# Kernel tuning notes

Hardware: AMD Instinct MI355X
Metric: run time of the kernel (lower is better)

The kernel has to match this reference:

```python
import jax, jax.numpy as jnp
import numpy as np

B, T, IN, H = 16, 4096, 512, 512


def gru_layer(x, W_ih, W_hh, b_ih, b_hh):
    """Single-layer batch_first GRU, torch gate ordering (r, z, n), h0 = 0.
    x: [B, T, IN]; W_ih: [3H, IN]; W_hh: [3H, H]; b_ih, b_hh: [3H].
    Returns outputs [B, T, H]."""
    Bn = x.shape[0]
    Hn = W_hh.shape[1]
    # input-side gate pre-activations computed once as a big GEMM
    xg = jnp.einsum('bti,gi->btg', x, W_ih) + b_ih  # [B, T, 3H]

    def step(h, xg_t):
        hg = h @ W_hh.T + b_hh  # [B, 3H]
        xr, xz, xn = jnp.split(xg_t, 3, axis=-1)
        hr, hz, hn = jnp.split(hg, 3, axis=-1)
        r = jax.nn.sigmoid(xr + hr)
        z = jax.nn.sigmoid(xz + hz)
        n = jnp.tanh(xn + r * hn)
        h_new = (1.0 - z) * n + z * h
        return h_new, h_new

    h0 = jnp.zeros((Bn, Hn), dtype=x.dtype)
    _, ys = jax.lax.scan(step, h0, jnp.swapaxes(xg, 0, 1))  # [T, B, H]
    return jnp.swapaxes(ys, 0, 1)


def setup_inputs() -> dict:
    key = jax.random.key(0)
    ks = jax.random.split(key, 9)
    s = 1.0 / np.sqrt(H)  # torch GRU init scale
    x = jax.random.normal(ks[0], (B, T, IN), dtype=jnp.float32)
    W_ih1 = jax.random.uniform(ks[1], (3 * H, IN), jnp.float32, -s, s)
    W_hh1 = jax.random.uniform(ks[2], (3 * H, H), jnp.float32, -s, s)
    b_ih1 = jax.random.uniform(ks[3], (3 * H,), jnp.float32, -s, s)
    b_hh1 = jax.random.uniform(ks[4], (3 * H,), jnp.float32, -s, s)
    W_ih2 = jax.random.uniform(ks[5], (3 * H, H), jnp.float32, -s, s)
    W_hh2 = jax.random.uniform(ks[6], (3 * H, H), jnp.float32, -s, s)
    b_ih2 = jax.random.uniform(ks[7], (3 * H,), jnp.float32, -s, s)
    b_hh2 = jax.random.uniform(ks[8], (3 * H,), jnp.float32, -s, s)
    return {"x": x, "W_ih1": W_ih1, "W_hh1": W_hh1, "b_ih1": b_ih1, "b_hh1": b_hh1,
            "W_ih2": W_ih2, "W_hh2": W_hh2, "b_ih2": b_ih2, "b_hh2": b_hh2}


def reference(x, W_ih1, W_hh1, b_ih1, b_hh1, W_ih2, W_hh2, b_ih2, b_hh2):
    y = gru_layer(x, W_ih1, W_hh1, b_ih1, b_hh1)  # rnn1
    z = gru_layer(y, W_ih2, W_hh2, b_ih2, b_hh2)  # rnn2
    return z + y  # residual skip around second GRU
```

## Files before the change

### kernel.cpp

```cpp
#include <hip/hip_runtime.h>
#include <hip/hip_bf16.h>


namespace {

constexpr int BATCH = 16;
constexpr int SEQ   = 4096;
constexpr int HD    = 512;
constexpr int NWG_L = 32;
constexpr int SLICE = 16;
constexpr int RING  = 8;
constexpr int BLK   = 6 * 64;

typedef short bf16x8 __attribute__((ext_vector_type(8)));
typedef float f32x4  __attribute__((ext_vector_type(4)));

__device__ __forceinline__ unsigned short f2bf(float f) {
  unsigned u = __float_as_uint(f);
  return (unsigned short)((u + 0x7fffu + ((u >> 16) & 1u)) >> 16);
}
__device__ __forceinline__ float bf2f(unsigned short s) {
  return __uint_as_float(((unsigned)s) << 16);
}

__device__ __forceinline__ void wait_ge(const unsigned* f, unsigned tgt) {
  while (__hip_atomic_load(f, __ATOMIC_RELAXED, __HIP_MEMORY_SCOPE_AGENT) < tgt) {}
}

#define MFMA16(a, b, c) __builtin_amdgcn_mfma_f32_16x16x32_bf16((a), (b), (c), 0, 0, 0)

__global__ __launch_bounds__(BLK, 1) void gru2_kernel(
    const float* __restrict__ x,
    const float* __restrict__ Wih1, const float* __restrict__ Whh1,
    const float* __restrict__ bih1, const float* __restrict__ bhh1,
    const float* __restrict__ Wih2, const float* __restrict__ Whh2,
    const float* __restrict__ bih2, const float* __restrict__ bhh2,
    float* __restrict__ out,
    unsigned* flags,
    unsigned short* ring)
{
  const int wg    = blockIdx.x;
  const int layer = wg >> 5;
  const int g     = wg & 31;
  const int tid   = threadIdx.x;
  const int w     = tid >> 6;
  const int lane  = tid & 63;
  const int nidx  = lane & 15;
  const int kgrp  = lane >> 4;

  __shared__ float gate_buf[6][16][16];
  __shared__ float h_own[16][16];

  const float* Wih = layer ? Wih2 : Wih1;
  const float* Whh = layer ? Whh2 : Whh1;
  const float* bih = layer ? bih2 : bih1;
  const float* bhh = layer ? bhh2 : bhh1;

  unsigned* flags1    = flags;
  unsigned* flags2    = flags + 32;
  unsigned* flags_own = layer ? flags2 : flags1;

  const unsigned short* ring1 = ring;
  unsigned short* ring_own = ring + (size_t)layer * (RING * BATCH * HD);

  if (tid < 256) h_own[tid >> 4][tid & 15] = 0.f;

  const int gate = (w < 3) ? w : (w - 3);
  const float* Wmat = (w < 3) ? Wih : Whh;
  const float* wrow = Wmat + ((size_t)gate * HD + (size_t)g * SLICE + nidx) * HD + kgrp * 8;
  bf16x8 bfrag[16];
  #pragma unroll
  for (int kk = 0; kk < 16; ++kk) {
    const float* p = wrow + kk * 32;
    bf16x8 f;
    #pragma unroll
    for (int i = 0; i < 8; ++i) f[i] = (short)f2bf(p[i]);
    bfrag[kk] = f;
  }

  float bi_r = 0, bi_z = 0, bi_n = 0, bh_r = 0, bh_z = 0, bh_n = 0;
  if (tid < 256) {
    int u = g * SLICE + (tid & 15);
    bi_r = bih[u]; bi_z = bih[HD + u]; bi_n = bih[2 * HD + u];
    bh_r = bhh[u]; bh_z = bhh[HD + u]; bh_n = bhh[2 * HD + u];
  }
  __syncthreads();

  for (int t = 0; t < SEQ; ++t) {
    f32x4 ac0 = {0.f,0.f,0.f,0.f}, ac1 = {0.f,0.f,0.f,0.f};
    f32x4 ac2 = {0.f,0.f,0.f,0.f}, ac3 = {0.f,0.f,0.f,0.f};

    if (w < 3) {
      if (layer == 0) {
        const float* px = x + ((size_t)nidx * SEQ + t) * HD + kgrp * 8;
        #pragma unroll
        for (int kk = 0; kk < 16; ++kk) {
          const float* p = px + kk * 32;
          bf16x8 a;
          #pragma unroll
          for (int i = 0; i < 8; ++i) a[i] = (short)f2bf(p[i]);
          if ((kk & 3) == 0)      ac0 = MFMA16(a, bfrag[kk], ac0);
          else if ((kk & 3) == 1) ac1 = MFMA16(a, bfrag[kk], ac1);
          else if ((kk & 3) == 2) ac2 = MFMA16(a, bfrag[kk], ac2);
          else                    ac3 = MFMA16(a, bfrag[kk], ac3);
        }
      } else {
        if (lane < 32) wait_ge(&flags1[lane], (unsigned)(t + 1));
        __builtin_amdgcn_fence(__ATOMIC_ACQUIRE, "agent");
        const unsigned short* py =
            ring1 + ((size_t)(t & (RING - 1)) * BATCH + nidx) * HD + kgrp * 8;
        #pragma unroll
        for (int kk = 0; kk < 16; ++kk) {
          bf16x8 a = *(const bf16x8*)(py + kk * 32);
          if ((kk & 3) == 0)      ac0 = MFMA16(a, bfrag[kk], ac0);
          else if ((kk & 3) == 1) ac1 = MFMA16(a, bfrag[kk], ac1);
          else if ((kk & 3) == 2) ac2 = MFMA16(a, bfrag[kk], ac2);
          else                    ac3 = MFMA16(a, bfrag[kk], ac3);
        }
      }
    } else {
      if (t > 0) {
        if (lane < 32) {
          wait_ge(&flags_own[lane], (unsigned)t);
        } else if (layer == 0 && t >= RING) {
          wait_ge(&flags2[lane - 32], (unsigned)(t - RING + 1));
        }
        __builtin_amdgcn_fence(__ATOMIC_ACQUIRE, "agent");
        const unsigned short* ph =
            ring_own + ((size_t)((t - 1) & (RING - 1)) * BATCH + nidx) * HD + kgrp * 8;
        #pragma unroll
        for (int kk = 0; kk < 16; ++kk) {
          bf16x8 a = *(const bf16x8*)(ph + kk * 32);
          if ((kk & 3) == 0)      ac0 = MFMA16(a, bfrag[kk], ac0);
          else if ((kk & 3) == 1) ac1 = MFMA16(a, bfrag[kk], ac1);
          else if ((kk & 3) == 2) ac2 = MFMA16(a, bfrag[kk], ac2);
          else                    ac3 = MFMA16(a, bfrag[kk], ac3);
        }
      }
    }

    f32x4 acc = (ac0 + ac1) + (ac2 + ac3);
    #pragma unroll
    for (int j = 0; j < 4; ++j) gate_buf[w][kgrp * 4 + j][nidx] = acc[j];
    __syncthreads();

    if (tid < 256) {
      const int b = tid >> 4, u = tid & 15;
      float rp = gate_buf[0][b][u] + bi_r + gate_buf[3][b][u] + bh_r;
      float zp = gate_buf[1][b][u] + bi_z + gate_buf[4][b][u] + bh_z;
      float xn = gate_buf[2][b][u] + bi_n;
      float hn = gate_buf[5][b][u] + bh_n;
      float r = 1.f / (1.f + __expf(-rp));
      float z = 1.f / (1.f + __expf(-zp));
      float n = tanhf(xn + r * hn);
      float hp = h_own[b][u];
      float hv = (1.f - z) * n + z * hp;
      h_own[b][u] = hv;
      ring_own[((size_t)(t & (RING - 1)) * BATCH + b) * HD + g * SLICE + u] = f2bf(hv);
      if (layer == 1) {
        float y = bf2f(ring1[((size_t)(t & (RING - 1)) * BATCH + b) * HD + g * SLICE + u]);
        out[((size_t)b * SEQ + t) * HD + g * SLICE + u] = hv + y;
      }
    }
    __syncthreads();
    if (tid == 0) {
      __builtin_amdgcn_fence(__ATOMIC_RELEASE, "agent");
      __hip_atomic_store(&flags_own[g], (unsigned)(t + 1),
                         __ATOMIC_RELAXED, __HIP_MEMORY_SCOPE_AGENT);
    }
  }
}

}

extern "C" void kernel_launch(void* const* d_in, const int* in_sizes, int n_in,
                              void* d_out, int out_size, void* d_ws, size_t ws_size,
                              hipStream_t stream) {
  const float* x    = (const float*)d_in[0];
  const float* Wih1 = (const float*)d_in[1];
  const float* Whh1 = (const float*)d_in[2];
  const float* bih1 = (const float*)d_in[3];
  const float* bhh1 = (const float*)d_in[4];
  const float* Wih2 = (const float*)d_in[5];
  const float* Whh2 = (const float*)d_in[6];
  const float* bih2 = (const float*)d_in[7];
  const float* bhh2 = (const float*)d_in[8];

  unsigned* flags = (unsigned*)d_ws;
  unsigned short* ring = (unsigned short*)((char*)d_ws + 1024);

  hipMemsetAsync(d_ws, 0, 1024, stream);

  gru2_kernel<<<dim3(2 * NWG_L), dim3(BLK), 0, stream>>>(
      x, Wih1, Whh1, bih1, bhh1, Wih2, Whh2, bih2, bhh2,
      (float*)d_out, flags, ring);
}
```

Measured before the change: 37.12 ms.

## Rewrite GRU pipeline with tagged-data rings, wider slices and LDS staging

Result: slower. 58.83 ms (+58.5%).

```diff
diff --git a/kernel.cpp b/kernel.cpp
--- a/kernel.cpp
+++ b/kernel.cpp
@@ -7,13 +7,16 @@
 constexpr int BATCH = 16;
 constexpr int SEQ   = 4096;
 constexpr int HD    = 512;
-constexpr int NWG_L = 32;
-constexpr int SLICE = 16;
-constexpr int RING  = 8;
-constexpr int BLK   = 6 * 64;
-
-typedef short bf16x8 __attribute__((ext_vector_type(8)));
-typedef float f32x4  __attribute__((ext_vector_type(4)));
+constexpr int NSLOT = 128;
+constexpr int NWGL  = 16;
+constexpr int SLICE = 32;
+constexpr int BLK   = 384;
+constexpr int SLOTU = BATCH * HD;
+
+typedef short    bf16x8 __attribute__((ext_vector_type(8)));
+typedef float    f32x4  __attribute__((ext_vector_type(4)));
+typedef unsigned u32x4  __attribute__((ext_vector_type(4)));
+typedef short    s16x4  __attribute__((ext_vector_type(4)));
 
 __device__ __forceinline__ unsigned short f2bf(float f) {
   unsigned u = __float_as_uint(f);
@@ -22,153 +25,285 @@
 __device__ __forceinline__ float bf2f(unsigned short s) {
   return __uint_as_float(((unsigned)s) << 16);
 }
-
-__device__ __forceinline__ void wait_ge(const unsigned* f, unsigned tgt) {
-  while (__hip_atomic_load(f, __ATOMIC_RELAXED, __HIP_MEMORY_SCOPE_AGENT) < tgt) {}
+__device__ __forceinline__ float sigm(float v) { return 1.f / (1.f + __expf(-v)); }
+__device__ __forceinline__ float tanh_(float v) { return 1.f - 2.f / (1.f + __expf(2.f * v)); }
+
+__device__ __forceinline__ void ld_u32_nw(unsigned* d, const unsigned* p) {
+  asm volatile("global_load_dword %0, %1, off sc0 sc1" : "=v"(*d) : "v"(p) : "memory");
+}
+__device__ __forceinline__ void ld_u32x4_nw(u32x4* d, const unsigned* p) {
+  asm volatile("global_load_dwordx4 %0, %1, off sc0 sc1" : "=v"(*d) : "v"(p) : "memory");
+}
+__device__ __forceinline__ void st_u32_sc(unsigned* p, unsigned v) {
+  asm volatile("global_store_dword %0, %1, off sc0 sc1" :: "v"(p), "v"(v) : "memory");
+}
+__device__ __forceinline__ void st_u32x4_sc(unsigned* p, u32x4 v) {
+  asm volatile("global_store_dwordx4 %0, %1, off sc0 sc1" :: "v"(p), "v"(v) : "memory");
+}
+__device__ __forceinline__ void vmwait0() {
+  asm volatile("s_waitcnt vmcnt(0)" ::: "memory");
+  __builtin_amdgcn_sched_barrier(0);
 }
 
 #define MFMA16(a, b, c) __builtin_amdgcn_mfma_f32_16x16x32_bf16((a), (b), (c), 0, 0, 0)
 
-__global__ __launch_bounds__(BLK, 1) void gru2_kernel(
+template <bool TWO>
+__device__ __forceinline__ void poll_stage(const unsigned* s0, unsigned t0, short* d0,
+                                           const unsigned* s1, unsigned t1, short* d1,
+                                           int tid) {
+  for (;;) {
+    unsigned sv[16];
+    #pragma unroll
+    for (int j = 0; j < 8; ++j) ld_u32_nw(&sv[j], s0 + j * 4 + 3);
+    if (TWO) {
+      #pragma unroll
+      for (int j = 0; j < 8; ++j) ld_u32_nw(&sv[8 + j], s1 + j * 4 + 3);
+    }
+    vmwait0();
+    unsigned bad = 0;
+    #pragma unroll
+    for (int j = 0; j < 8; ++j) bad |= (sv[j] ^ t0) & 0xffffu;
+    if (TWO) {
+      #pragma unroll
+      for (int j = 0; j < 8; ++j) bad |= (sv[8 + j] ^ t1) & 0xffffu;
+    }
+    if (!bad) break;
+    __builtin_amdgcn_s_sleep(1);
+  }
+  u32x4 v0[8], v1[8];
+  for (;;) {
+    #pragma unroll
+    for (int j = 0; j < 8; ++j) ld_u32x4_nw(&v0[j], s0 + j * 4);
+    if (TWO) {
+      #pragma unroll
+      for (int j = 0; j < 8; ++j) ld_u32x4_nw(&v1[j], s1 + j * 4);
+    }
+    vmwait0();
+    unsigned bad = 0;
+    #pragma unroll
+    for (int j = 0; j < 8; ++j)
+      #pragma unroll
+      for (int e = 0; e < 4; ++e) bad |= (v0[j][e] ^ t0) & 0xffffu;
+    if (TWO) {
+      #pragma unroll
+      for (int j = 0; j < 8; ++j)
+        #pragma unroll
+        for (int e = 0; e < 4; ++e) bad |= (v1[j][e] ^ t1) & 0xffffu;
+    }
+    if (!bad) break;
+    __builtin_amdgcn_s_sleep(1);
+  }
+  const int row = tid >> 4, kb2 = (tid & 15) * 64, sz = (row & 7) << 4;
+  #pragma unroll
+  for (int blk = 0; blk < 4; ++blk) {
+    const u32x4 a = v0[blk * 2], b = v0[blk * 2 + 1];
+    u32x4 p;
+    p[0] = (a[0] >> 16) | (a[1] & 0xffff0000u);
+    p[1] = (a[2] >> 16) | (a[3] & 0xffff0000u);
+    p[2] = (b[0] >> 16) | (b[1] & 0xffff0000u);
+    p[3] = (b[2] >> 16) | (b[3] & 0xffff0000u);
+    *(u32x4*)((char*)d0 + row * 1024 + ((kb2 + blk * 16) ^ sz)) = p;
+  }
+  if (TWO) {
+    #pragma unroll
+    for (int blk = 0; blk < 4; ++blk) {
+      const u32x4 a = v1[blk * 2], b = v1[blk * 2 + 1];
+      u32x4 p;
+      p[0] = (a[0] >> 16) | (a[1] & 0xffff0000u);
+      p[1] = (a[2] >> 16) | (a[3] & 0xffff0000u);
+      p[2] = (b[0] >> 16) | (b[1] & 0xffff0000u);
+      p[3] = (b[2] >> 16) | (b[3] & 0xffff0000u);
+      *(u32x4*)((char*)d1 + row * 1024 + ((kb2 + blk * 16) ^ sz)) = p;
+    }
+  }
+}
+
+template <int LAYER>
+__device__ void layer_fn(const float* __restrict__ x,
+                         const float* __restrict__ Wih, const float* __restrict__ Whh,
+                         const float* __restrict__ bih, const float* __restrict__ bhh,
+                         float* __restrict__ out,
+                         unsigned* l2prog, unsigned* yring, unsigned* ownring,
+                         int s, char* smem) {
+  const int tid = threadIdx.x, w = tid >> 6, lane = tid & 63;
+  const int c = lane & 15, q = lane >> 4;
+
+  short* hstage = (short*)smem;
+  short* ystage = (short*)(smem + 32768);
+  float* gbI = (float*)(smem + 65536);
+  float* gbH = (float*)(smem + 77824);
+  float* hf  = (float*)(smem + 90112);
+  float* biasI = (float*)(smem + 92672);
+  float* biasH = (float*)(smem + 93056);
+
+  for (int i = tid; i < 16 * 40; i += BLK) hf[i] = 0.f;
+  if (tid < 96) {
+    int g = tid >> 5, u = tid & 31;
+    int r = g * HD + s * SLICE + u;
+    biasI[tid] = bih[r];
+    biasH[tid] = bhh[r];
+  }
+
+  const int rowb = (w >> 1) * HD + s * SLICE + (w & 1) * 16;
+  bf16x8 wfi[16], wfh[16];
+  {
+    const float* pi = Wih + (size_t)(rowb + c) * HD + q * 8;
+    const float* ph = Whh + (size_t)(rowb + c) * HD + q * 8;
+    #pragma unroll
+    for (int kk = 0; kk < 16; ++kk) {
+      bf16x8 fi, fh;
+      #pragma unroll
+      for (int i = 0; i < 8; ++i) {
+        fi[i] = (short)f2bf(pi[kk * 32 + i]);
+        fh[i] = (short)f2bf(ph[kk * 32 + i]);
+      }
+      wfi[kk] = fi;
+      wfh[kk] = fh;
+    }
+  }
+  __syncthreads();
+
+  for (int t = 0; t < SEQ; ++t) {
+    const int slot = t & (NSLOT - 1), pslot = (t - 1) & (NSLOT - 1), buf = t & 1;
+
+    if (LAYER == 0) {
+      if (tid == 0 && t >= NSLOT && (t & 63) == 0) {
+        const unsigned need = (unsigned)(t - 64);
+        for (;;) {
+          unsigned pv[NWGL];
+          #pragma unroll
+          for (int i = 0; i < NWGL; ++i) ld_u32_nw(&pv[i], &l2prog[i]);
+          vmwait0();
+          unsigned m = 0xffffffffu;
+          #pragma unroll
+          for (int i = 0; i < NWGL; ++i) m = pv[i] < m ? pv[i] : m;
+          if (m >= need) break;
+          __builtin_amdgcn_s_sleep(16);
+        }
+      }
+    } else {
+      if (tid == BLK - 1) st_u32_sc(&l2prog[s], (unsigned)t);
+    }
+
+    if (tid < 256) {
+      if (LAYER == 0) {
+        if (t > 0)
+          poll_stage<false>(ownring + (size_t)pslot * SLOTU + tid * 32, (unsigned)t,
+                            hstage + buf * 8192, nullptr, 0, nullptr, tid);
+      } else {
+        if (t > 0)
+          poll_stage<true>(ownring + (size_t)pslot * SLOTU + tid * 32, (unsigned)t,
+                           hstage + buf * 8192,
+                           yring + (size_t)slot * SLOTU + tid * 32, (unsigned)(t + 1),
+                           ystage + buf * 8192, tid);
+        else
+          poll_stage<false>(yring + (size_t)slot * SLOTU + tid * 32, (unsigned)(t + 1),
+                            ystage + buf * 8192, nullptr, 0, nullptr, tid);
+      }
+    }
+    __syncthreads();
+
+    f32x4 aI0 = {0.f,0.f,0.f,0.f}, aI1 = {0.f,0.f,0.f,0.f};
+    f32x4 aH0 = {0.f,0.f,0.f,0.f}, aH1 = {0.f,0.f,0.f,0.f};
+    if (LAYER == 0) {
+      const float* px = x + ((size_t)c * SEQ + t) * HD + q * 8;
+      #pragma unroll
+      for (int blk = 0; blk < 4; ++blk) {
+        f32x4 xa[8];
+        #pragma unroll
+        for (int f = 0; f < 4; ++f) {
+          xa[2 * f]     = *(const f32x4*)(px + (blk * 4 + f) * 32);
+          xa[2 * f + 1] = *(const f32x4*)(px + (blk * 4 + f) * 32 + 4);
+        }
+        #pragma unroll
+        for (int f = 0; f < 4; ++f) {
+          bf16x8 a;
+          #pragma unroll
+          for (int i = 0; i < 4; ++i) {
+            a[i]     = (short)f2bf(xa[2 * f][i]);
+            a[4 + i] = (short)f2bf(xa[2 * f + 1][i]);
+          }
+          if (f & 1) aI1 = MFMA16(a, wfi[blk * 4 + f], aI1);
+          else       aI0 = MFMA16(a, wfi[blk * 4 + f], aI0);
+        }
+      }
+    } else {
+      const char* yb = (const char*)(ystage + buf * 8192);
+      #pragma unroll
+      for (int kk = 0; kk < 16; ++kk) {
+        bf16x8 a = *(const bf16x8*)(yb + c * 1024 + ((kk * 64 + q * 16) ^ ((c & 7) << 4)));
+        if (kk & 1) aI1 = MFMA16(a, wfi[kk], aI1);
+        else        aI0 = MFMA16(a, wfi[kk], aI0);
+      }
+    }
+    if (t > 0) {
+      const char* hb = (const char*)(hstage + buf * 8192);
+      #pragma unroll
+      for (int kk = 0; kk < 16; ++kk) {
+        bf16x8 a = *(const bf16x8*)(hb + c * 1024 + ((kk * 64 + q * 16) ^ ((c & 7) << 4)));
+        if (kk & 1) aH1 = MFMA16(a, wfh[kk], aH1);
+        else        aH0 = MFMA16(a, wfh[kk], aH0);
+      }
+    }
+    {
+      f32x4 aI = aI0 + aI1, aH = aH0 + aH1;
+      float* gI = gbI + (buf * 6 + w) * 256;
+      float* gH = gbH + (buf * 6 + w) * 256;
+      #pragma unroll
+      for (int j = 0; j < 4; ++j) {
+        gI[(q * 4 + j) * 16 + c] = aI[j];
+        gH[(q * 4 + j) * 16 + c] = aH[j];
+      }
+    }
+    __syncthreads();
+
+    if (tid < 128) {
+      const int b = tid >> 3, u0 = (tid & 7) * 4;
+      u32x4 pk;
+      f32x4 hv4;
+      #pragma unroll
+      for (int jj = 0; jj < 4; ++jj) {
+        const int u = u0 + jj, half = u >> 4, n = u & 15;
+        const int oR = ((buf * 6 + half) * 16 + b) * 16 + n;
+        const int oZ = ((buf * 6 + 2 + half) * 16 + b) * 16 + n;
+        const int oN = ((buf * 6 + 4 + half) * 16 + b) * 16 + n;
+        float r = sigm(gbI[oR] + gbH[oR] + biasI[u] + biasH[u]);
+        float z = sigm(gbI[oZ] + gbH[oZ] + biasI[32 + u] + biasH[32 + u]);
+        float pn = gbI[oN] + biasI[64 + u] + r * (gbH[oN] + biasH[64 + u]);
+        float nn = tanh_(pn);
+        float hp = hf[b * 40 + u];
+        float hv = (1.f - z) * nn + z * hp;
+        hf[b * 40 + u] = hv;
+        hv4[jj] = hv;
+        pk[jj] = ((unsigned)f2bf(hv) << 16) | (unsigned)(t + 1);
+      }
+      st_u32x4_sc(ownring + (size_t)slot * SLOTU + b * HD + s * SLICE + u0, pk);
+      if (LAYER == 1) {
+        const char* yb = (const char*)(ystage + buf * 8192);
+        s16x4 yv = *(const s16x4*)(yb + b * 1024 + (((s * SLICE + u0) * 2) ^ ((b & 7) << 4)));
+        f32x4 o;
+        #pragma unroll
+        for (int jj = 0; jj < 4; ++jj) o[jj] = hv4[jj] + bf2f((unsigned short)yv[jj]);
+        *(f32x4*)(out + ((size_t)b * SEQ + t) * HD + s * SLICE + u0) = o;
+      }
+    }
+  }
+}
+
+__global__ __launch_bounds__(BLK, 2) void gru2_k(
     const float* __restrict__ x,
     const float* __restrict__ Wih1, const float* __restrict__ Whh1,
     const float* __restrict__ bih1, const float* __restrict__ bhh1,
     const float* __restrict__ Wih2, const float* __restrict__ Whh2,
     const float* __restrict__ bih2, const float* __restrict__ bhh2,
     float* __restrict__ out,
-    unsigned* flags,
-    unsigned short* ring)
-{
-  const int wg    = blockIdx.x;
-  const int layer = wg >> 5;
-  const int g     = wg & 31;
-  const int tid   = threadIdx.x;
-  const int w     = tid >> 6;
-  const int lane  = tid & 63;
-  const int nidx  = lane & 15;
-  const int kgrp  = lane >> 4;
-
-  __shared__ float gate_buf[6][16][16];
-  __shared__ float h_own[16][16];
-
-  const float* Wih = layer ? Wih2 : Wih1;
-  const float* Whh = layer ? Whh2 : Whh1;
-  const float* bih = layer ? bih2 : bih1;
-  const float* bhh = layer ? bhh2 : bhh1;
-
-  unsigned* flags1    = flags;
-  unsigned* flags2    = flags + 32;
-  unsigned* flags_own = layer ? flags2 : flags1;
-
-  const unsigned short* ring1 = ring;
-  unsigned short* ring_own = ring + (size_t)layer * (RING * BATCH * HD);
-
-  if (tid < 256) h_own[tid >> 4][tid & 15] = 0.f;
-
-  const int gate = (w < 3) ? w : (w - 3);
-  const float* Wmat = (w < 3) ? Wih : Whh;
-  const float* wrow = Wmat + ((size_t)gate * HD + (size_t)g * SLICE + nidx) * HD + kgrp * 8;
-  bf16x8 bfrag[16];
-  #pragma unroll
-  for (int kk = 0; kk < 16; ++kk) {
-    const float* p = wrow + kk * 32;
-    bf16x8 f;
-    #pragma unroll
-    for (int i = 0; i < 8; ++i) f[i] = (short)f2bf(p[i]);
-    bfrag[kk] = f;
-  }
-
-  float bi_r = 0, bi_z = 0, bi_n = 0, bh_r = 0, bh_z = 0, bh_n = 0;
-  if (tid < 256) {
-    int u = g * SLICE + (tid & 15);
-    bi_r = bih[u]; bi_z = bih[HD + u]; bi_n = bih[2 * HD + u];
-    bh_r = bhh[u]; bh_z = bhh[HD + u]; bh_n = bhh[2 * HD + u];
-  }
-  __syncthreads();
-
-  for (int t = 0; t < SEQ; ++t) {
-    f32x4 ac0 = {0.f,0.f,0.f,0.f}, ac1 = {0.f,0.f,0.f,0.f};
-    f32x4 ac2 = {0.f,0.f,0.f,0.f}, ac3 = {0.f,0.f,0.f,0.f};
-
-    if (w < 3) {
-      if (layer == 0) {
-        const float* px = x + ((size_t)nidx * SEQ + t) * HD + kgrp * 8;
-        #pragma unroll
-        for (int kk = 0; kk < 16; ++kk) {
-          const float* p = px + kk * 32;
-          bf16x8 a;
-          #pragma unroll
-          for (int i = 0; i < 8; ++i) a[i] = (short)f2bf(p[i]);
-          if ((kk & 3) == 0)      ac0 = MFMA16(a, bfrag[kk], ac0);
-          else if ((kk & 3) == 1) ac1 = MFMA16(a, bfrag[kk], ac1);
-          else if ((kk & 3) == 2) ac2 = MFMA16(a, bfrag[kk], ac2);
-          else                    ac3 = MFMA16(a, bfrag[kk], ac3);
-        }
-      } else {
-        if (lane < 32) wait_ge(&flags1[lane], (unsigned)(t + 1));
-        __builtin_amdgcn_fence(__ATOMIC_ACQUIRE, "agent");
-        const unsigned short* py =
-            ring1 + ((size_t)(t & (RING - 1)) * BATCH + nidx) * HD + kgrp * 8;
-        #pragma unroll
-        for (int kk = 0; kk < 16; ++kk) {
-          bf16x8 a = *(const bf16x8*)(py + kk * 32);
-          if ((kk & 3) == 0)      ac0 = MFMA16(a, bfrag[kk], ac0);
-          else if ((kk & 3) == 1) ac1 = MFMA16(a, bfrag[kk], ac1);
-          else if ((kk & 3) == 2) ac2 = MFMA16(a, bfrag[kk], ac2);
-          else                    ac3 = MFMA16(a, bfrag[kk], ac3);
-        }
-      }
-    } else {
-      if (t > 0) {
-        if (lane < 32) {
-          wait_ge(&flags_own[lane], (unsigned)t);
-        } else if (layer == 0 && t >= RING) {
-          wait_ge(&flags2[lane - 32], (unsigned)(t - RING + 1));
-        }
-        __builtin_amdgcn_fence(__ATOMIC_ACQUIRE, "agent");
-        const unsigned short* ph =
-            ring_own + ((size_t)((t - 1) & (RING - 1)) * BATCH + nidx) * HD + kgrp * 8;
-        #pragma unroll
-        for (int kk = 0; kk < 16; ++kk) {
-          bf16x8 a = *(const bf16x8*)(ph + kk * 32);
-          if ((kk & 3) == 0)      ac0 = MFMA16(a, bfrag[kk], ac0);
-          else if ((kk & 3) == 1) ac1 = MFMA16(a, bfrag[kk], ac1);
-          else if ((kk & 3) == 2) ac2 = MFMA16(a, bfrag[kk], ac2);
-          else                    ac3 = MFMA16(a, bfrag[kk], ac3);
-        }
-      }
-    }
-
-    f32x4 acc = (ac0 + ac1) + (ac2 + ac3);
-    #pragma unroll
-    for (int j = 0; j < 4; ++j) gate_buf[w][kgrp * 4 + j][nidx] = acc[j];
-    __syncthreads();
-
-    if (tid < 256) {
-      const int b = tid >> 4, u = tid & 15;
-      float rp = gate_buf[0][b][u] + bi_r + gate_buf[3][b][u] + bh_r;
-      float zp = gate_buf[1][b][u] + bi_z + gate_buf[4][b][u] + bh_z;
-      float xn = gate_buf[2][b][u] + bi_n;
-      float hn = gate_buf[5][b][u] + bh_n;
-      float r = 1.f / (1.f + __expf(-rp));
-      float z = 1.f / (1.f + __expf(-zp));
-      float n = tanhf(xn + r * hn);
-      float hp = h_own[b][u];
-      float hv = (1.f - z) * n + z * hp;
-      h_own[b][u] = hv;
-      ring_own[((size_t)(t & (RING - 1)) * BATCH + b) * HD + g * SLICE + u] = f2bf(hv);
-      if (layer == 1) {
-        float y = bf2f(ring1[((size_t)(t & (RING - 1)) * BATCH + b) * HD + g * SLICE + u]);
-        out[((size_t)b * SEQ + t) * HD + g * SLICE + u] = hv + y;
-      }
-    }
-    __syncthreads();
-    if (tid == 0) {
-      __builtin_amdgcn_fence(__ATOMIC_RELEASE, "agent");
-      __hip_atomic_store(&flags_own[g], (unsigned)(t + 1),
-                         __ATOMIC_RELAXED, __HIP_MEMORY_SCOPE_AGENT);
-    }
-  }
+    unsigned* l2prog, unsigned* yring, unsigned* h2ring) {
+  __shared__ char smem[93440];
+  const int bx = blockIdx.x;
+  if (bx < NWGL)
+    layer_fn<0>(x, Wih1, Whh1, bih1, bhh1, out, l2prog, yring, yring, bx, smem);
+  else
+    layer_fn<1>(x, Wih2, Whh2, bih2, bhh2, out, l2prog, yring, h2ring, bx - NWGL, smem);
 }
 
 }
@@ -186,12 +321,13 @@
   const float* bih2 = (const float*)d_in[7];
   const float* bhh2 = (const float*)d_in[8];
 
-  unsigned* flags = (unsigned*)d_ws;
-  unsigned short* ring = (unsigned short*)((char*)d_ws + 1024);
-
-  hipMemsetAsync(d_ws, 0, 1024, stream);
-
-  gru2_kernel<<<dim3(2 * NWG_L), dim3(BLK), 0, stream>>>(
+  unsigned* l2prog = (unsigned*)d_ws;
+  unsigned* yring  = (unsigned*)((char*)d_ws + 4096);
+  unsigned* h2ring = yring + (size_t)NSLOT * SLOTU;
+
+  hipMemsetAsync(d_ws, 0, 256, stream);
+
+  gru2_k<<<dim3(2 * NWGL), dim3(BLK), 0, stream>>>(
       x, Wih1, Whh1, bih1, bhh1, Wih2, Whh2, bih2, bhh2,
-      (float*)d_out, flags, ring);
-}
+      (float*)d_out, l2prog, yring, h2ring);
+}
```
